# Optimization experiments

Hardware: AMD Instinct MI355X
Metric: run time of the kernel (lower is better)

## Reference

```python
import jax, jax.numpy as jnp
import numpy as np

N, C_IN, H, W = 32, 128, 56, 56
C_OUT, K = 256, 3
STRIDE = (1, 1)
PAD = (1, 1)


def setup_inputs() -> dict:
    key = jax.random.key(0)
    kx, kw = jax.random.split(key)
    x = jax.random.normal(kx, (N, C_IN, H, W), dtype=jnp.float32)
    k = 1.0 / np.sqrt(C_IN * K * K)
    kernels = jax.random.uniform(kw, (C_OUT, C_IN, K, K), dtype=jnp.float32) * (2 * k) - k
    return {"x": x, "kernels": kernels}


def reference(x, kernels):
    # Equivalent to the im2col + matmul conv in the source (zero padding,
    # stride 1, no bias added in the original forward).
    out = jax.lax.conv_general_dilated(
        x, kernels,
        window_strides=STRIDE,
        padding=[(PAD[0], PAD[0]), (PAD[1], PAD[1])],
        dimension_numbers=("NCHW", "OIHW", "NCHW"),
    )
    return out  # (N, C_OUT, H_out, W_out)
```

## Files before the change

kernel.cpp:

```cpp
#include <hip/hip_runtime.h>


#define CIN   128
#define COUT  256
#define HWID  56
#define IMG   (HWID*HWID)
#define NIMG  32
#define CSTR  40
#define BROW  (58*CSTR)

typedef __attribute__((ext_vector_type(8))) short short8;
typedef __attribute__((ext_vector_type(4))) float float4v;

__device__ __forceinline__ unsigned short f2bf(float f) {
    unsigned int u = __builtin_bit_cast(unsigned int, f);
    u += 0x7FFFu + ((u >> 16) & 1u);
    return (unsigned short)(u >> 16);
}

__global__ void prep_w_kernel(const float* __restrict__ w, unsigned short* __restrict__ W2) {
    int o = blockIdx.x * 256 + threadIdx.x;
    int ci_lo = o & 31;
    int co    = (o >> 5) & 255;
    int s     = o >> 13;
    int ci_hi = s / 9;
    int r9    = s - ci_hi * 9;
    W2[o] = f2bf(w[(co * CIN + ci_hi * 32 + ci_lo) * 9 + r9]);
}

__global__ void prep_x_kernel(const float* __restrict__ x, unsigned short* __restrict__ X2) {
    __shared__ unsigned short Ls[32 * 65];
    int b  = blockIdx.x;
    int pb = b % 49;
    int t  = b / 49;
    int cb = t & 3;
    int n  = t >> 2;
    int p0 = pb * 64, ci0 = cb * 32;

    const float* src = x + ((long)n * CIN + ci0) * IMG + p0;
    #pragma unroll
    for (int it = 0; it < 8; ++it) {
        int flat = it * 256 + threadIdx.x;
        int ci_l = flat >> 6, p_l = flat & 63;
        Ls[ci_l * 65 + p_l] = f2bf(src[ci_l * IMG + p_l]);
    }
    __syncthreads();
    unsigned short* dst = X2 + ((long)n * IMG + p0) * CIN + ci0;
    #pragma unroll
    for (int it = 0; it < 8; ++it) {
        int flat = it * 256 + threadIdx.x;
        int ci_l = flat & 31, p_l = flat >> 5;
        dst[(long)p_l * CIN + ci_l] = Ls[ci_l * 65 + p_l];
    }
}

__global__ __launch_bounds__(256, 2)
void conv_mfma_kernel(const unsigned short* __restrict__ X2,
                      const unsigned short* __restrict__ W2,
                      float* __restrict__ out) {
    __shared__ __align__(16) unsigned short Bs[4 * BROW];

    const int tid  = threadIdx.x;
    const int lane = tid & 63;
    const int wv   = tid >> 6;
    const int l15  = lane & 15;
    const int quad = lane >> 4;

    const int pt    = blockIdx.x;
    const int n_img = pt / 28;
    const int h0    = (pt % 28) * 2;

    int boff[7];
    #pragma unroll
    for (int n = 0; n < 7; ++n) {
        int p    = n * 16 + l15;
        int prow = (p >= 56) ? 1 : 0;
        int pcol = p - prow * 56;
        boff[n]  = (prow * 58 + pcol) * CSTR + quad * 8;
    }

    const unsigned short* wbase = W2 + (wv * 64 + l15) * 32 + quad * 8;

    float4v acc[4][7];
    #pragma unroll
    for (int m = 0; m < 4; ++m)
        #pragma unroll
        for (int n = 0; n < 7; ++n)
            acc[m][n] = (float4v){0.f, 0.f, 0.f, 0.f};

    const unsigned short* xnb = X2 + (long)n_img * (IMG * CIN);

    for (int ci_hi = 0; ci_hi < 4; ++ci_hi) {
        __syncthreads();

        #pragma unroll
        for (int it = 0; it < 4; ++it) {
            int idx = it * 256 + tid;
            int ci8 = idx & 3;
            int rc  = idx >> 2;
            if (rc < 232) {
                int r = rc / 58;
                int c = rc - r * 58;
                int h = h0 - 1 + r;
                int w = c - 1;
                uint4 v = make_uint4(0u, 0u, 0u, 0u);
                if ((unsigned)h < 56u && (unsigned)w < 56u)
                    v = *(const uint4*)(xnb + ((h * HWID + w) * CIN + ci_hi * 32 + ci8 * 8));
                *(uint4*)(&Bs[rc * CSTR + ci8 * 8]) = v;
            }
        }
        __syncthreads();

        #pragma unroll
        for (int khw = 0; khw < 9; ++khw) {
            const int kh = khw / 3, kw = khw - (khw / 3) * 3;
            const int step = ci_hi * 9 + khw;
            short8 a[4], b[7];
            #pragma unroll
            for (int m = 0; m < 4; ++m)
                a[m] = *(const short8*)(wbase + step * 8192 + m * 512);
            #pragma unroll
            for (int n = 0; n < 7; ++n)
                b[n] = *(const short8*)(&Bs[boff[n] + (kh * 58 + kw) * CSTR]);
            #pragma unroll
            for (int m = 0; m < 4; ++m)
                #pragma unroll
                for (int n = 0; n < 7; ++n)
                    acc[m][n] = __builtin_amdgcn_mfma_f32_16x16x32_bf16(a[m], b[n], acc[m][n], 0, 0, 0);
        }
    }

    float* obase = out + (long)n_img * (COUT * IMG) + h0 * HWID;
    #pragma unroll
    for (int m = 0; m < 4; ++m) {
        #pragma unroll
        for (int r = 0; r < 4; ++r) {
            int co = wv * 64 + m * 16 + quad * 4 + r;
            float* orow = obase + (long)co * IMG;
            #pragma unroll
            for (int n = 0; n < 7; ++n)
                orow[n * 16 + l15] = acc[m][n][r];
        }
    }
}

extern "C" void kernel_launch(void* const* d_in, const int* in_sizes, int n_in,
                              void* d_out, int out_size, void* d_ws, size_t ws_size,
                              hipStream_t stream) {
    const float* x  = (const float*)d_in[0];
    const float* wt = (const float*)d_in[1];
    float* out = (float*)d_out;

    unsigned short* X2 = (unsigned short*)d_ws;
    unsigned short* W2 = X2 + (long)NIMG * CIN * IMG;

    prep_x_kernel<<<NIMG * 4 * 49, 256, 0, stream>>>(x, X2);
    prep_w_kernel<<<(COUT * CIN * 9) / 256, 256, 0, stream>>>(wt, W2);
    conv_mfma_kernel<<<896, 256, 0, stream>>>(X2, W2, out);
}
```

Before: 207.0 us.

## Prefetch next input tile into registers during MFMA loop; vectorize input prep

The conv kernel now loads the next channel-chunk tile from global memory into registers before running the current chunk's MFMA loop, then writes it to LDS at the top of the next iteration. The goal is to hide global-load latency behind compute instead of stalling between LDS fills. The input prep kernel also switches to float4 reads and 16-byte packed bf16 writes, with padding to reduce bank conflicts. The cost is 16 extra VGPRs per thread holding the prefetched tile, which could pressure occupancy under the launch bound of 2 blocks per SM.

```diff
diff --git a/kernel.cpp b/kernel.cpp
--- a/kernel.cpp
+++ b/kernel.cpp
@@ -28,8 +28,9 @@
     W2[o] = f2bf(w[(co * CIN + ci_hi * 32 + ci_lo) * 9 + r9]);
 }
 
-__global__ void prep_x_kernel(const float* __restrict__ x, unsigned short* __restrict__ X2) {
-    __shared__ unsigned short Ls[32 * 65];
+__global__ __launch_bounds__(256) void prep_x_kernel(const float* __restrict__ x,
+                                                     unsigned short* __restrict__ X2) {
+    __shared__ unsigned short Ls[32 * 66];
     int b  = blockIdx.x;
     int pb = b % 49;
     int t  = b / 49;
@@ -39,20 +40,45 @@
 
     const float* src = x + ((long)n * CIN + ci0) * IMG + p0;
     #pragma unroll
-    for (int it = 0; it < 8; ++it) {
+    for (int it = 0; it < 2; ++it) {
         int flat = it * 256 + threadIdx.x;
-        int ci_l = flat >> 6, p_l = flat & 63;
-        Ls[ci_l * 65 + p_l] = f2bf(src[ci_l * IMG + p_l]);
+        int ci_l = flat >> 4;
+        int c4   = flat & 15;
+        float4 v = *(const float4*)(src + ci_l * IMG + c4 * 4);
+        unsigned int lo = (unsigned int)f2bf(v.x) | ((unsigned int)f2bf(v.y) << 16);
+        unsigned int hi = (unsigned int)f2bf(v.z) | ((unsigned int)f2bf(v.w) << 16);
+        *(unsigned int*)(&Ls[ci_l * 66 + c4 * 4])     = lo;
+        *(unsigned int*)(&Ls[ci_l * 66 + c4 * 4 + 2]) = hi;
     }
     __syncthreads();
+    int p_l = threadIdx.x >> 2;
+    int c8  = threadIdx.x & 3;
     unsigned short* dst = X2 + ((long)n * IMG + p0) * CIN + ci0;
+    short8 o;
     #pragma unroll
-    for (int it = 0; it < 8; ++it) {
-        int flat = it * 256 + threadIdx.x;
-        int ci_l = flat & 31, p_l = flat >> 5;
-        dst[(long)p_l * CIN + ci_l] = Ls[ci_l * 65 + p_l];
-    }
+    for (int j = 0; j < 8; ++j)
+        o[j] = (short)Ls[(c8 * 8 + j) * 66 + p_l];
+    *(short8*)(&dst[(long)p_l * CIN + c8 * 8]) = o;
 }
+
+#define ISSUE_TILE(CIHI) do {                                                   \
+    _Pragma("unroll")                                                           \
+    for (int it = 0; it < 4; ++it) {                                            \
+        int idx = it * 256 + tid;                     \
+        int ci8 = idx & 3;                                                      \
+        int rc  = idx >> 2;                          \
+        uint4 v = make_uint4(0u, 0u, 0u, 0u);                                   \
+        if (rc < 232) {                                                         \
+            int r = rc / 58;                                                    \
+            int c = rc - r * 58;                                                \
+            int h = h0 - 1 + r;                                                 \
+            int w = c - 1;                                                      \
+            if ((unsigned)h < 56u && (unsigned)w < 56u)                         \
+                v = *(const uint4*)(xnb + ((h * HWID + w) * CIN + (CIHI) * 32 + ci8 * 8)); \
+        }                                                                       \
+        rx[it] = v;                                                             \
+    }                                                                           \
+} while (0)
 
 __global__ __launch_bounds__(256, 2)
 void conv_mfma_kernel(const unsigned short* __restrict__ X2,
@@ -90,43 +116,41 @@
 
     const unsigned short* xnb = X2 + (long)n_img * (IMG * CIN);
 
+    uint4 rx[4];
+    ISSUE_TILE(0);
+
     for (int ci_hi = 0; ci_hi < 4; ++ci_hi) {
         __syncthreads();
 
         #pragma unroll
         for (int it = 0; it < 4; ++it) {
             int idx = it * 256 + tid;
-            int ci8 = idx & 3;
             int rc  = idx >> 2;
             if (rc < 232) {
-                int r = rc / 58;
-                int c = rc - r * 58;
-                int h = h0 - 1 + r;
-                int w = c - 1;
-                uint4 v = make_uint4(0u, 0u, 0u, 0u);
-                if ((unsigned)h < 56u && (unsigned)w < 56u)
-                    v = *(const uint4*)(xnb + ((h * HWID + w) * CIN + ci_hi * 32 + ci8 * 8));
-                *(uint4*)(&Bs[rc * CSTR + ci8 * 8]) = v;
+                int ci8 = idx & 3;
+                *(uint4*)(&Bs[rc * CSTR + ci8 * 8]) = rx[it];
             }
         }
         __syncthreads();
+
+        if (ci_hi < 3) ISSUE_TILE(ci_hi + 1);
 
         #pragma unroll
         for (int khw = 0; khw < 9; ++khw) {
             const int kh = khw / 3, kw = khw - (khw / 3) * 3;
             const int step = ci_hi * 9 + khw;
-            short8 a[4], b[7];
+            short8 a[4], bfr[7];
             #pragma unroll
             for (int m = 0; m < 4; ++m)
                 a[m] = *(const short8*)(wbase + step * 8192 + m * 512);
             #pragma unroll
             for (int n = 0; n < 7; ++n)
-                b[n] = *(const short8*)(&Bs[boff[n] + (kh * 58 + kw) * CSTR]);
+                bfr[n] = *(const short8*)(&Bs[boff[n] + (kh * 58 + kw) * CSTR]);
             #pragma unroll
             for (int m = 0; m < 4; ++m)
                 #pragma unroll
                 for (int n = 0; n < 7; ++n)
-                    acc[m][n] = __builtin_amdgcn_mfma_f32_16x16x32_bf16(a[m], b[n], acc[m][n], 0, 0, 0);
+                    acc[m][n] = __builtin_amdgcn_mfma_f32_16x16x32_bf16(a[m], bfr[n], acc[m][n], 0, 0, 0);
         }
     }
 
```

Measured after the change: 205.0 us. Within noise of the previous version (-0.9%).

## Fuse input transpose and bf16 conversion into conv kernel, stage all channels in LDS

Applied to the files above, without the earlier changes.

Removes the separate prep_x kernel and instead has the conv kernel read fp32 NCHW rows directly, convert them to bf16 and transpose them through a small per-wave LDS buffer into a full 128-channel halo tile. The intent is to drop the global round trip through the transposed intermediate buffer and the per-channel-chunk syncthreads. It also software-prefetches the next weight fragments, remaps block indices, and changes LDS stride to 32, which may add bank conflicts. Staging all channels at once raises LDS use, which could limit occupancy.

```diff
diff --git a/kernel.cpp b/kernel.cpp
--- a/kernel.cpp
+++ b/kernel.cpp
@@ -6,8 +6,8 @@
 #define HWID  56
 #define IMG   (HWID*HWID)
 #define NIMG  32
-#define CSTR  40
-#define BROW  (58*CSTR)
+#define XP    32
+#define XCH   (232*XP)
 
 typedef __attribute__((ext_vector_type(8))) short short8;
 typedef __attribute__((ext_vector_type(4))) float float4v;
@@ -18,7 +18,8 @@
     return (unsigned short)(u >> 16);
 }
 
-__global__ void prep_w_kernel(const float* __restrict__ w, unsigned short* __restrict__ W2) {
+__global__ __launch_bounds__(256) void prep_w_kernel(const float* __restrict__ w,
+                                                     unsigned short* __restrict__ W2) {
     int o = blockIdx.x * 256 + threadIdx.x;
     int ci_lo = o & 31;
     int co    = (o >> 5) & 255;
@@ -28,37 +29,12 @@
     W2[o] = f2bf(w[(co * CIN + ci_hi * 32 + ci_lo) * 9 + r9]);
 }
 
-__global__ void prep_x_kernel(const float* __restrict__ x, unsigned short* __restrict__ X2) {
-    __shared__ unsigned short Ls[32 * 65];
-    int b  = blockIdx.x;
-    int pb = b % 49;
-    int t  = b / 49;
-    int cb = t & 3;
-    int n  = t >> 2;
-    int p0 = pb * 64, ci0 = cb * 32;
-
-    const float* src = x + ((long)n * CIN + ci0) * IMG + p0;
-    #pragma unroll
-    for (int it = 0; it < 8; ++it) {
-        int flat = it * 256 + threadIdx.x;
-        int ci_l = flat >> 6, p_l = flat & 63;
-        Ls[ci_l * 65 + p_l] = f2bf(src[ci_l * IMG + p_l]);
-    }
-    __syncthreads();
-    unsigned short* dst = X2 + ((long)n * IMG + p0) * CIN + ci0;
-    #pragma unroll
-    for (int it = 0; it < 8; ++it) {
-        int flat = it * 256 + threadIdx.x;
-        int ci_l = flat & 31, p_l = flat >> 5;
-        dst[(long)p_l * CIN + ci_l] = Ls[ci_l * 65 + p_l];
-    }
-}
-
 __global__ __launch_bounds__(256, 2)
-void conv_mfma_kernel(const unsigned short* __restrict__ X2,
+void conv_mfma_kernel(const float* __restrict__ x,
                       const unsigned short* __restrict__ W2,
                       float* __restrict__ out) {
-    __shared__ __align__(16) unsigned short Bs[4 * BROW];
+    __shared__ __align__(16) unsigned short Xs[4 * XCH];
+    __shared__ unsigned short Ls[4][8 * 66];
 
     const int tid  = threadIdx.x;
     const int lane = tid & 63;
@@ -66,9 +42,48 @@
     const int l15  = lane & 15;
     const int quad = lane >> 4;
 
-    const int pt    = blockIdx.x;
+    const int pt    = (blockIdx.x & 7) * 112 + (blockIdx.x >> 3);
     const int n_img = pt / 28;
     const int h0    = (pt % 28) * 2;
+
+    {
+        const int h    = h0 - 1 + wv;
+        const bool hval = ((unsigned)h < 56u);
+        unsigned short* Lw = &Ls[wv][0];
+        const float* xrow = x + (long)n_img * (CIN * IMG) + h * HWID;
+
+        #pragma unroll 2
+        for (int ci8 = 0; ci8 < 16; ++ci8) {
+            if (hval) {
+                #pragma unroll
+                for (int i = 0; i < 2; ++i) {
+                    int flat = i * 64 + lane;
+                    int cl   = flat >> 4;
+                    int c4   = flat & 15;
+                    if (c4 < 14) {
+                        float4 v = *(const float4*)(xrow + ((long)(ci8 * 8 + cl)) * IMG + c4 * 4);
+                        unsigned int lo = (unsigned int)f2bf(v.x) | ((unsigned int)f2bf(v.y) << 16);
+                        unsigned int hi = (unsigned int)f2bf(v.z) | ((unsigned int)f2bf(v.w) << 16);
+                        *(unsigned int*)(&Lw[cl * 66 + c4 * 4])     = lo;
+                        *(unsigned int*)(&Lw[cl * 66 + c4 * 4 + 2]) = hi;
+                    }
+                }
+            }
+            int p_l = lane;
+            if (p_l < 58) {
+                short8 o = (short8){0,0,0,0,0,0,0,0};
+                if (hval && p_l > 0 && p_l < 57) {
+                    #pragma unroll
+                    for (int j = 0; j < 8; ++j)
+                        o[j] = (short)Lw[j * 66 + (p_l - 1)];
+                }
+                int rc    = wv * 58 + p_l;
+                int ci_hi = ci8 >> 2;
+                *(short8*)(&Xs[ci_hi * XCH + rc * XP + (ci8 & 3) * 8]) = o;
+            }
+        }
+    }
+    __syncthreads();
 
     int boff[7];
     #pragma unroll
@@ -76,7 +91,7 @@
         int p    = n * 16 + l15;
         int prow = (p >= 56) ? 1 : 0;
         int pcol = p - prow * 56;
-        boff[n]  = (prow * 58 + pcol) * CSTR + quad * 8;
+        boff[n]  = (prow * 58 + pcol) * XP + quad * 8;
     }
 
     const unsigned short* wbase = W2 + (wv * 64 + l15) * 32 + quad * 8;
@@ -88,45 +103,36 @@
         for (int n = 0; n < 7; ++n)
             acc[m][n] = (float4v){0.f, 0.f, 0.f, 0.f};
 
-    const unsigned short* xnb = X2 + (long)n_img * (IMG * CIN);
+    short8 a[4], an[4];
+    #pragma unroll
+    for (int m = 0; m < 4; ++m)
+        a[m] = *(const short8*)(wbase + m * 512);
 
+    #pragma unroll
     for (int ci_hi = 0; ci_hi < 4; ++ci_hi) {
-        __syncthreads();
-
-        #pragma unroll
-        for (int it = 0; it < 4; ++it) {
-            int idx = it * 256 + tid;
-            int ci8 = idx & 3;
-            int rc  = idx >> 2;
-            if (rc < 232) {
-                int r = rc / 58;
-                int c = rc - r * 58;
-                int h = h0 - 1 + r;
-                int w = c - 1;
-                uint4 v = make_uint4(0u, 0u, 0u, 0u);
-                if ((unsigned)h < 56u && (unsigned)w < 56u)
-                    v = *(const uint4*)(xnb + ((h * HWID + w) * CIN + ci_hi * 32 + ci8 * 8));
-                *(uint4*)(&Bs[rc * CSTR + ci8 * 8]) = v;
-            }
-        }
-        __syncthreads();
-
         #pragma unroll
         for (int khw = 0; khw < 9; ++khw) {
+            const int step = ci_hi * 9 + khw;
             const int kh = khw / 3, kw = khw - (khw / 3) * 3;
-            const int step = ci_hi * 9 + khw;
-            short8 a[4], b[7];
-            #pragma unroll
-            for (int m = 0; m < 4; ++m)
-                a[m] = *(const short8*)(wbase + step * 8192 + m * 512);
+            if (step < 35) {
+                #pragma unroll
+                for (int m = 0; m < 4; ++m)
+                    an[m] = *(const short8*)(wbase + (step + 1) * 8192 + m * 512);
+            }
+            short8 bfr[7];
             #pragma unroll
             for (int n = 0; n < 7; ++n)
-                b[n] = *(const short8*)(&Bs[boff[n] + (kh * 58 + kw) * CSTR]);
+                bfr[n] = *(const short8*)(&Xs[ci_hi * XCH + boff[n] + (kh * 58 + kw) * XP]);
             #pragma unroll
             for (int m = 0; m < 4; ++m)
                 #pragma unroll
                 for (int n = 0; n < 7; ++n)
-                    acc[m][n] = __builtin_amdgcn_mfma_f32_16x16x32_bf16(a[m], b[n], acc[m][n], 0, 0, 0);
+                    acc[m][n] = __builtin_amdgcn_mfma_f32_16x16x32_bf16(a[m], bfr[n], acc[m][n], 0, 0, 0);
+            if (step < 35) {
+                #pragma unroll
+                for (int m = 0; m < 4; ++m)
+                    a[m] = an[m];
+            }
         }
     }
 
@@ -151,10 +157,8 @@
     const float* wt = (const float*)d_in[1];
     float* out = (float*)d_out;
 
-    unsigned short* X2 = (unsigned short*)d_ws;
-    unsigned short* W2 = X2 + (long)NIMG * CIN * IMG;
+    unsigned short* W2 = (unsigned short*)d_ws;
 
-    prep_x_kernel<<<NIMG * 4 * 49, 256, 0, stream>>>(x, X2);
     prep_w_kernel<<<(COUT * CIN * 9) / 256, 256, 0, stream>>>(wt, W2);
-    conv_mfma_kernel<<<896, 256, 0, stream>>>(X2, W2, out);
+    conv_mfma_kernel<<<NIMG * 28, 256, 0, stream>>>(x, W2, out);
 }
```

Result: faster. 189.8 us (-8.3%).
